# Performance work log

Measured on AMD Instinct MI355X. Metric: run time of the kernel, lower is better.

Reference implementation:

```python
import jax, jax.numpy as jnp
import numpy as np

# Fixed by JastrowNet source: ElectronicSchNet(n_interactions=2, kernel_dim=8, embedding_dim=16, version=1)
BATCH = 512
N_UP, N_DOWN = 16, 16
N_ELEC = N_UP + N_DOWN
N_ATOMS = 8
DIST_FEAT = 32
KERNEL = 8
EMBED = 16
N_LAYERS = 2
W_HIDDEN = 16  # log-spaced hidden dim of the w filter MLP: round(sqrt(32*8))
N_CHAN = 3     # same-spin, anti-spin, nuclear filter channels


def ssp(x):
    # shifted softplus used by SchNet
    return jax.nn.softplus(x) - jnp.log(2.0).astype(x.dtype)


def setup_inputs() -> dict:
    key = jax.random.key(0)
    ks = jax.random.split(key, 16)
    s = lambda fan_in: 1.0 / np.sqrt(fan_in)
    inp = {
        # Gaussian-expanded distance features are non-negative
        'edges_elec': jax.random.uniform(ks[0], (BATCH, N_ELEC, N_ELEC, DIST_FEAT), jnp.float32),
        'edges_nuc': jax.random.uniform(ks[1], (BATCH, N_ELEC, N_ATOMS, DIST_FEAT), jnp.float32),
        # electron spin embedding table (up=0, down=1) and nuclear embeddings Y
        'X_emb': jax.random.normal(ks[2], (2, EMBED), jnp.float32),
        'Y': jax.random.normal(ks[3], (N_ATOMS, KERNEL), jnp.float32),
        # per-layer, per-channel w filter MLP (dist_feat -> hidden -> kernel)
        'wW1': jax.random.normal(ks[4], (N_LAYERS, N_CHAN, DIST_FEAT, W_HIDDEN), jnp.float32) * s(DIST_FEAT),
        'wb1': jnp.zeros((N_LAYERS, N_CHAN, W_HIDDEN), jnp.float32),
        'wW2': jax.random.normal(ks[5], (N_LAYERS, N_CHAN, W_HIDDEN, KERNEL), jnp.float32) * s(W_HIDDEN),
        'wb2': jnp.zeros((N_LAYERS, N_CHAN, KERNEL), jnp.float32),
        # per-layer h subnet (embed -> kernel) and g subnet (kernel -> embed)
        'hW': jax.random.normal(ks[6], (N_LAYERS, EMBED, KERNEL), jnp.float32) * s(EMBED),
        'hb': jnp.zeros((N_LAYERS, KERNEL), jnp.float32),
        'gW': jax.random.normal(ks[7], (N_LAYERS, KERNEL, EMBED), jnp.float32) * s(KERNEL),
        'gb': jnp.zeros((N_LAYERS, EMBED), jnp.float32),
        # readout: Linear(16, 1, bias=False)
        'orb_W': jax.random.normal(ks[8], (EMBED,), jnp.float32) * s(EMBED),
    }
    return inp


def reference(edges_elec, edges_nuc, X_emb, Y, wW1, wb1, wW2, wb2, hW, hb, gW, gb, orb_W):
    B = edges_elec.shape[0]
    spins = jnp.concatenate([jnp.zeros(N_UP, jnp.int32), jnp.ones(N_DOWN, jnp.int32)])
    not_self = ~jnp.eye(N_ELEC, dtype=bool)
    same = ((spins[:, None] == spins[None, :]) & not_self)  # [n,n]
    anti = (spins[:, None] != spins[None, :])

    # initial electron embeddings by spin, broadcast over batch
    x = jnp.broadcast_to(X_emb[spins], (B, N_ELEC, EMBED))

    for l in range(N_LAYERS):
        def w_sub(e, c):
            h1 = ssp(e @ wW1[l, c] + wb1[l, c])
            return ssp(h1 @ wW2[l, c] + wb2[l, c])  # [..., KERNEL]

        w_same = w_sub(edges_elec, 0) * same[None, :, :, None]  # [B,n,n,k]
        w_anti = w_sub(edges_elec, 1) * anti[None, :, :, None]
        w_n = w_sub(edges_nuc, 2)                                # [B,n,m,k]

        hx = ssp(x @ hW[l] + hb[l])                              # [B,n,k]
        # continuous-filter message passing: gather neighbor features, multiply by filter, scatter-sum
        z = jnp.einsum('bijk,bjk->bik', w_same + w_anti, hx)
        z = z + jnp.einsum('bimk,mk->bik', w_n, Y)
        # version 1: single g applied to combined message, residual update
        x = x + z @ gW[l] + gb[l]

    # orbital readout Linear(16,1,bias=False).squeeze(-1).sum(-1)
    return (x @ orb_W).sum(axis=-1)  # [B]
```

## Files before the change

kernel.cpp:

```cpp
#include <hip/hip_runtime.h>
#include <hip/hip_bf16.h>
#include <cstddef>
#include <cstdint>


#define NB   512
#define NE   32
#define NA   8
#define NF   32
#define NH   16
#define NK   8
#define NEMB 16

typedef __attribute__((ext_vector_type(8))) short short8;
typedef __attribute__((ext_vector_type(4))) float f32x4;

__device__ __forceinline__ float ssp(float v){
    return fmaxf(v, 0.f) + __logf(1.f + __expf(-fabsf(v))) - 0.6931471805599453f;
}

__device__ __forceinline__ short f2bf(float x){
    unsigned b = __float_as_uint(x);
    b += 0x7fffu + ((b >> 16) & 1u);
    return (short)(b >> 16);
}
__device__ __forceinline__ unsigned packbf2(float lo, float hi){
    return (unsigned)(unsigned short)f2bf(lo) | ((unsigned)(unsigned short)f2bf(hi) << 16);
}
__device__ __forceinline__ short8 cvt_row(float4 a, float4 b){
    short8 s;
    s[0]=f2bf(a.x); s[1]=f2bf(a.y); s[2]=f2bf(a.z); s[3]=f2bf(a.w);
    s[4]=f2bf(b.x); s[5]=f2bf(b.y); s[6]=f2bf(b.z); s[7]=f2bf(b.w);
    return s;
}

extern "C" __global__ void __launch_bounds__(512, 4)
jastrow_kernel(const float* __restrict__ edges_elec,
               const float* __restrict__ edges_nuc,
               const float* __restrict__ X_emb,
               const float* __restrict__ Yk,
               const float* __restrict__ wW1, const float* __restrict__ wb1,
               const float* __restrict__ wW2, const float* __restrict__ wb2,
               const float* __restrict__ hW,  const float* __restrict__ hb,
               const float* __restrict__ gW,  const float* __restrict__ gb,
               const float* __restrict__ orbW,
               float* __restrict__ out)
{
    __shared__ __align__(16) __hip_bfloat16 s_w2[NE*NE*NK];
    __shared__ __align__(16) float s_z1p[2*NE*NK];
    __shared__ __align__(16) float s_zn1[NE*NK];
    __shared__ __align__(16) float s_zn2[NE*NK];
    __shared__ float s_hx1[2*NK];
    __shared__ float s_x[NE*NEMB];
    __shared__ float s_z[NE*NK];
    __shared__ float s_hx[NE*NK];
    __shared__ float s_red[8];

    const int b = blockIdx.x, t = threadIdx.x;
    const int wid = t >> 6, lane = t & 63;
    const int r16 = lane & 15, g4 = lane >> 4;

    if (t < 2*NK){
        const int s = t >> 3, k = t & 7;
        float acc = hb[k];
#pragma unroll
        for (int e = 0; e < NEMB; e++)
            acc = fmaf(X_emb[s*NEMB + e], hW[e*NK + k], acc);
        s_hx1[t] = ssp(acc);
    }
    __syncthreads();

    const int s0 = (g4*32 + r16) & 63;
    const int s1 = (g4*32 + 16 + r16) & 63;

    auto build = [&](int cc, short8* a1, short8* a2, f32x4* c1, f32x4* c2){
#pragma unroll
        for (int l = 0; l < 2; l++){
            const float* W1 = wW1 + (size_t)(l*3 + cc)*NF*NH;
            const float* W2 = wW2 + (size_t)(l*3 + cc)*NH*NK;
            short8 s, s2;
#pragma unroll
            for (int e = 0; e < 8; e++){
                s[e] = f2bf(W1[(g4*8 + e)*NH + r16]);
                const int h = g4*8 + e;
                s2[e] = (h < NH && r16 < NK) ? f2bf(W2[h*NK + r16]) : (short)0;
            }
            a1[l] = s; a2[l] = s2;
            const float* B1 = wb1 + (l*3 + cc)*NH;
            const float* B2 = wb2 + (l*3 + cc)*NK;
            f32x4 cb1, cb2;
#pragma unroll
            for (int r = 0; r < 4; r++){
                const int m = g4*4 + r;
                cb1[r] = B1[m];
                cb2[r] = (m < NK) ? B2[m] : 0.f;
            }
            c1[l] = cb1; c2[l] = cb2;
        }
    };

#pragma unroll
    for (int cc = 0; cc < 2; cc++){
        short8 a1[2], a2[2]; f32x4 c1[2], c2[2];
        build(cc, a1, a2, c1, c2);
#pragma unroll
        for (int u = 0; u < 4; u++){
            const int tau = wid*4 + u;
            const int qi = tau >> 4;
            const int qj = cc ? (1 - qi) : qi;
            const int g  = tau & 15;
            const int i  = qi*16 + g;
            const float* src = edges_elec
                + (((size_t)b*NE + i)*NE + qj*16 + r16)*NF + g4*8;
            const float4 ra = ((const float4*)src)[0];
            const float4 rb = ((const float4*)src)[1];
            const short8 bfr = cvt_row(ra, rb);
#pragma unroll
            for (int l = 0; l < 2; l++){
                f32x4 d1 = __builtin_amdgcn_mfma_f32_16x16x32_bf16(a1[l], bfr, c1[l], 0, 0, 0);
                const unsigned p0 = packbf2(ssp(d1[0]), ssp(d1[1]));
                const unsigned p1 = packbf2(ssp(d1[2]), ssp(d1[3]));
                unsigned q0 = __shfl(p0, s0, 64);
                unsigned q1 = __shfl(p1, s0, 64);
                unsigned q2 = __shfl(p0, s1, 64);
                unsigned q3 = __shfl(p1, s1, 64);
                if (g4 >= 2){ q0 = 0u; q1 = 0u; q2 = 0u; q3 = 0u; }
                union { unsigned u4[4]; short8 v; } bb;
                bb.u4[0]=q0; bb.u4[1]=q1; bb.u4[2]=q2; bb.u4[3]=q3;
                f32x4 d2 = __builtin_amdgcn_mfma_f32_16x16x32_bf16(a2[l], bb.v, c2[l], 0, 0, 0);
                float wk[4];
#pragma unroll
                for (int r = 0; r < 4; r++) wk[r] = ssp(d2[r]);
                if (cc == 0 && r16 == g){
#pragma unroll
                    for (int r = 0; r < 4; r++) wk[r] = 0.f;
                }
                if (l == 0){
#pragma unroll
                    for (int off = 1; off < 16; off <<= 1)
#pragma unroll
                        for (int r = 0; r < 4; r++) wk[r] += __shfl_xor(wk[r], off, 64);
                    if (r16 == 0 && g4 < 2){
                        float4 st;
                        st.x = wk[0]*s_hx1[qj*NK + g4*4 + 0];
                        st.y = wk[1]*s_hx1[qj*NK + g4*4 + 1];
                        st.z = wk[2]*s_hx1[qj*NK + g4*4 + 2];
                        st.w = wk[3]*s_hx1[qj*NK + g4*4 + 3];
                        *(float4*)&s_z1p[(qj*NE + i)*NK + g4*4] = st;
                    }
                } else if (g4 < 2){
                    const int j = qj*16 + r16;
                    uint2 uu;
                    uu.x = packbf2(wk[0], wk[1]);
                    uu.y = packbf2(wk[2], wk[3]);
                    *(uint2*)&s_w2[(i*NE + j)*NK + g4*4] = uu;
                }
            }
        }
    }

    {
        short8 a1[2], a2[2]; f32x4 c1[2], c2[2];
        build(2, a1, a2, c1, c2);
        const int m = lane & 7;
        float Yv[4];
#pragma unroll
        for (int r = 0; r < 4; r++)
            Yv[r] = Yk[m*NK + ((g4*4 + r) & 7)];
#pragma unroll
        for (int u = 0; u < 2; u++){
            const int gp = wid*2 + u;
            const int i  = 2*gp + (r16 >> 3);
            const float* src = edges_nuc
                + (((size_t)b*NE + i)*NA + m)*NF + g4*8;
            const float4 ra = ((const float4*)src)[0];
            const float4 rb = ((const float4*)src)[1];
            const short8 bfr = cvt_row(ra, rb);
#pragma unroll
            for (int l = 0; l < 2; l++){
                f32x4 d1 = __builtin_amdgcn_mfma_f32_16x16x32_bf16(a1[l], bfr, c1[l], 0, 0, 0);
                const unsigned p0 = packbf2(ssp(d1[0]), ssp(d1[1]));
                const unsigned p1 = packbf2(ssp(d1[2]), ssp(d1[3]));
                unsigned q0 = __shfl(p0, s0, 64);
                unsigned q1 = __shfl(p1, s0, 64);
                unsigned q2 = __shfl(p0, s1, 64);
                unsigned q3 = __shfl(p1, s1, 64);
                if (g4 >= 2){ q0 = 0u; q1 = 0u; q2 = 0u; q3 = 0u; }
                union { unsigned u4[4]; short8 v; } bb;
                bb.u4[0]=q0; bb.u4[1]=q1; bb.u4[2]=q2; bb.u4[3]=q3;
                f32x4 d2 = __builtin_amdgcn_mfma_f32_16x16x32_bf16(a2[l], bb.v, c2[l], 0, 0, 0);
                float wk[4];
#pragma unroll
                for (int r = 0; r < 4; r++) wk[r] = ssp(d2[r]) * Yv[r];
#pragma unroll
                for (int off = 1; off < 8; off <<= 1)
#pragma unroll
                    for (int r = 0; r < 4; r++) wk[r] += __shfl_xor(wk[r], off, 64);
                if ((r16 & 7) == 0 && g4 < 2){
                    float* dst = l ? s_zn2 : s_zn1;
                    float4 st; st.x = wk[0]; st.y = wk[1]; st.z = wk[2]; st.w = wk[3];
                    *(float4*)&dst[i*NK + g4*4] = st;
                }
            }
        }
    }
    __syncthreads();

    if (t < NE*NK)
        s_z[t] = s_z1p[t] + s_z1p[NE*NK + t] + s_zn1[t];
    __syncthreads();
    {
        const int i = t >> 4, e = t & 15;
        float acc = gb[e];
#pragma unroll
        for (int k = 0; k < NK; k++)
            acc = fmaf(s_z[i*NK + k], gW[k*NEMB + e], acc);
        s_x[t] = X_emb[(i >> 4)*NEMB + e] + acc;
    }
    __syncthreads();
    if (t < NE*NK){
        const int i = t >> 3, k = t & 7;
        float acc = hb[NK + k];
#pragma unroll
        for (int e = 0; e < NEMB; e++)
            acc = fmaf(s_x[i*NEMB + e], hW[NEMB*NK + e*NK + k], acc);
        s_hx[t] = ssp(acc);
    }
    __syncthreads();
    {
        const int i = t >> 4, j16 = t & 15;
        float zacc[NK];
#pragma unroll
        for (int k = 0; k < NK; k++) zacc[k] = 0.f;
#pragma unroll
        for (int qj = 0; qj < 2; qj++){
            const int j = qj*16 + j16;
            union { uint4 u; __hip_bfloat16 h[8]; } raw;
            raw.u = *(const uint4*)&s_w2[((size_t)i*NE + j)*NK];
            float pk[NK];
#pragma unroll
            for (int k = 0; k < NK; k++)
                pk[k] = __bfloat162float(raw.h[k]) * s_hx[j*NK + k];
#pragma unroll
            for (int off = 8; off > 0; off >>= 1)
#pragma unroll
                for (int k = 0; k < NK; k++) pk[k] += __shfl_down(pk[k], off, 16);
#pragma unroll
            for (int k = 0; k < NK; k++) zacc[k] += pk[k];
        }
        if (j16 == 0){
#pragma unroll
            for (int k = 0; k < NK; k++)
                s_z[i*NK + k] = zacc[k] + s_zn2[i*NK + k];
        }
    }
    __syncthreads();
    {
        const int i = t >> 4, e = t & 15;
        float acc = gb[NEMB + e];
#pragma unroll
        for (int k = 0; k < NK; k++)
            acc = fmaf(s_z[i*NK + k], gW[NK*NEMB + k*NEMB + e], acc);
        s_x[t] += acc;
    }
    __syncthreads();
    float part = s_x[t] * orbW[t & 15];
#pragma unroll
    for (int off = 32; off > 0; off >>= 1) part += __shfl_down(part, off, 64);
    if (lane == 0) s_red[wid] = part;
    __syncthreads();
    if (t == 0){
        float r = 0.f;
#pragma unroll
        for (int w = 0; w < 8; w++) r += s_red[w];
        out[b] = r;
    }
}

extern "C" void kernel_launch(void* const* d_in, const int* in_sizes, int n_in,
                              void* d_out, int out_size, void* d_ws, size_t ws_size,
                              hipStream_t stream)
{
    const float* edges_elec = (const float*)d_in[0];
    const float* edges_nuc  = (const float*)d_in[1];
    const float* X_emb      = (const float*)d_in[2];
    const float* Yk         = (const float*)d_in[3];
    const float* wW1        = (const float*)d_in[4];
    const float* wb1        = (const float*)d_in[5];
    const float* wW2        = (const float*)d_in[6];
    const float* wb2        = (const float*)d_in[7];
    const float* hW         = (const float*)d_in[8];
    const float* hb         = (const float*)d_in[9];
    const float* gW         = (const float*)d_in[10];
    const float* gb         = (const float*)d_in[11];
    const float* orbW       = (const float*)d_in[12];

    jastrow_kernel<<<NB, 512, 0, stream>>>(
        edges_elec, edges_nuc, X_emb, Yk, wW1, wb1, wW2, wb2, hW, hb,
        gW, gb, orbW, (float*)d_out);
}
```

Baseline: 156.2 us.

## Double block size, split filter channels across waves, use 16x16x16 second MFMA

Launches 1024 threads per block, with each wave handling a single electron filter channel. Each wave now processes four electron rows for one channel, and the nuclear pass covers one row pair. The second filter layer switches to the 16x16x16 bf16 MFMA, fed directly from per-lane ssp outputs, which removes the cross-lane shuffles and zero-padding that the K=32 instruction needed. The intent is more parallelism per batch item and fewer shuffle and ALU ops. The cost is more idle threads in the later per-electron phases and a larger block that may limit occupancy.

```diff
diff --git a/kernel.cpp b/kernel.cpp
--- a/kernel.cpp
+++ b/kernel.cpp
@@ -13,6 +13,7 @@
 #define NEMB 16
 
 typedef __attribute__((ext_vector_type(8))) short short8;
+typedef __attribute__((ext_vector_type(4))) short short4b;
 typedef __attribute__((ext_vector_type(4))) float f32x4;
 
 __device__ __forceinline__ float ssp(float v){
@@ -34,7 +35,18 @@
     return s;
 }
 
-extern "C" __global__ void __launch_bounds__(512, 4)
+__device__ __forceinline__ f32x4 mfma16x16(short4b a, short4b b, f32x4 c){
+#if __has_builtin(__builtin_amdgcn_mfma_f32_16x16x16bf16_1k)
+    return __builtin_amdgcn_mfma_f32_16x16x16bf16_1k(a, b, c, 0, 0, 0);
+#else
+    f32x4 d;
+    asm("s_nop 1\n\tv_mfma_f32_16x16x16_bf16 %0, %1, %2, %3\n\ts_nop 7"
+        : "=v"(d) : "v"(a), "v"(b), "v"(c));
+    return d;
+#endif
+}
+
+extern "C" __global__ void __launch_bounds__(1024, 8)
 jastrow_kernel(const float* __restrict__ edges_elec,
                const float* __restrict__ edges_nuc,
                const float* __restrict__ X_emb,
@@ -54,7 +66,7 @@
     __shared__ float s_x[NE*NEMB];
     __shared__ float s_z[NE*NK];
     __shared__ float s_hx[NE*NK];
-    __shared__ float s_red[8];
+    __shared__ float s_red[16];
 
     const int b = blockIdx.x, t = threadIdx.x;
     const int wid = t >> 6, lane = t & 63;
@@ -70,22 +82,22 @@
     }
     __syncthreads();
 
-    const int s0 = (g4*32 + r16) & 63;
-    const int s1 = (g4*32 + 16 + r16) & 63;
-
-    auto build = [&](int cc, short8* a1, short8* a2, f32x4* c1, f32x4* c2){
+    short8 a1[2]; short4b a2[2]; f32x4 c1[2], c2[2];
+    auto build = [&](int cc){
 #pragma unroll
         for (int l = 0; l < 2; l++){
             const float* W1 = wW1 + (size_t)(l*3 + cc)*NF*NH;
             const float* W2 = wW2 + (size_t)(l*3 + cc)*NH*NK;
-            short8 s, s2;
-#pragma unroll
-            for (int e = 0; e < 8; e++){
+            short8 s;
+#pragma unroll
+            for (int e = 0; e < 8; e++)
                 s[e] = f2bf(W1[(g4*8 + e)*NH + r16]);
-                const int h = g4*8 + e;
-                s2[e] = (h < NH && r16 < NK) ? f2bf(W2[h*NK + r16]) : (short)0;
-            }
-            a1[l] = s; a2[l] = s2;
+            a1[l] = s;
+            short4b s2;
+#pragma unroll
+            for (int e = 0; e < 4; e++)
+                s2[e] = (r16 < NK) ? f2bf(W2[(g4*4 + e)*NK + r16]) : (short)0;
+            a2[l] = s2;
             const float* B1 = wb1 + (l*3 + cc)*NH;
             const float* B2 = wb2 + (l*3 + cc)*NK;
             f32x4 cb1, cb2;
@@ -99,108 +111,92 @@
         }
     };
 
-#pragma unroll
-    for (int cc = 0; cc < 2; cc++){
-        short8 a1[2], a2[2]; f32x4 c1[2], c2[2];
-        build(cc, a1, a2, c1, c2);
-#pragma unroll
-        for (int u = 0; u < 4; u++){
-            const int tau = wid*4 + u;
-            const int qi = tau >> 4;
-            const int qj = cc ? (1 - qi) : qi;
-            const int g  = tau & 15;
-            const int i  = qi*16 + g;
-            const float* src = edges_elec
-                + (((size_t)b*NE + i)*NE + qj*16 + r16)*NF + g4*8;
-            const float4 ra = ((const float4*)src)[0];
-            const float4 rb = ((const float4*)src)[1];
-            const short8 bfr = cvt_row(ra, rb);
-#pragma unroll
-            for (int l = 0; l < 2; l++){
-                f32x4 d1 = __builtin_amdgcn_mfma_f32_16x16x32_bf16(a1[l], bfr, c1[l], 0, 0, 0);
-                const unsigned p0 = packbf2(ssp(d1[0]), ssp(d1[1]));
-                const unsigned p1 = packbf2(ssp(d1[2]), ssp(d1[3]));
-                unsigned q0 = __shfl(p0, s0, 64);
-                unsigned q1 = __shfl(p1, s0, 64);
-                unsigned q2 = __shfl(p0, s1, 64);
-                unsigned q3 = __shfl(p1, s1, 64);
-                if (g4 >= 2){ q0 = 0u; q1 = 0u; q2 = 0u; q3 = 0u; }
-                union { unsigned u4[4]; short8 v; } bb;
-                bb.u4[0]=q0; bb.u4[1]=q1; bb.u4[2]=q2; bb.u4[3]=q3;
-                f32x4 d2 = __builtin_amdgcn_mfma_f32_16x16x32_bf16(a2[l], bb.v, c2[l], 0, 0, 0);
-                float wk[4];
-#pragma unroll
-                for (int r = 0; r < 4; r++) wk[r] = ssp(d2[r]);
-                if (cc == 0 && r16 == g){
-#pragma unroll
-                    for (int r = 0; r < 4; r++) wk[r] = 0.f;
+    const int ccE = wid & 1;
+    const int wq  = (wid >> 1) * 4;
+    build(ccE);
+#pragma unroll
+    for (int u = 0; u < 4; u++){
+        const int tau = wq + u;
+        const int qi = tau >> 4, g = tau & 15;
+        const int qj = ccE ? (1 - qi) : qi;
+        const int i  = qi*16 + g;
+        const float* src = edges_elec
+            + (((size_t)b*NE + i)*NE + qj*16 + r16)*NF + g4*8;
+        const float4 ra = ((const float4*)src)[0];
+        const float4 rb = ((const float4*)src)[1];
+        const short8 bfr = cvt_row(ra, rb);
+#pragma unroll
+        for (int l = 0; l < 2; l++){
+            f32x4 d1 = __builtin_amdgcn_mfma_f32_16x16x32_bf16(a1[l], bfr, c1[l], 0, 0, 0);
+            short4b bb;
+            bb[0] = f2bf(ssp(d1[0]));
+            bb[1] = f2bf(ssp(d1[1]));
+            bb[2] = f2bf(ssp(d1[2]));
+            bb[3] = f2bf(ssp(d1[3]));
+            f32x4 d2 = mfma16x16(a2[l], bb, c2[l]);
+            float wk[4];
+#pragma unroll
+            for (int r = 0; r < 4; r++) wk[r] = ssp(d2[r]);
+            if (ccE == 0 && r16 == g){
+#pragma unroll
+                for (int r = 0; r < 4; r++) wk[r] = 0.f;
+            }
+            if (l == 0){
+#pragma unroll
+                for (int off = 1; off < 16; off <<= 1)
+#pragma unroll
+                    for (int r = 0; r < 4; r++) wk[r] += __shfl_xor(wk[r], off, 64);
+                if (r16 == 0 && g4 < 2){
+                    float4 st;
+                    st.x = wk[0]*s_hx1[qj*NK + g4*4 + 0];
+                    st.y = wk[1]*s_hx1[qj*NK + g4*4 + 1];
+                    st.z = wk[2]*s_hx1[qj*NK + g4*4 + 2];
+                    st.w = wk[3]*s_hx1[qj*NK + g4*4 + 3];
+                    *(float4*)&s_z1p[(qj*NE + i)*NK + g4*4] = st;
                 }
-                if (l == 0){
-#pragma unroll
-                    for (int off = 1; off < 16; off <<= 1)
-#pragma unroll
-                        for (int r = 0; r < 4; r++) wk[r] += __shfl_xor(wk[r], off, 64);
-                    if (r16 == 0 && g4 < 2){
-                        float4 st;
-                        st.x = wk[0]*s_hx1[qj*NK + g4*4 + 0];
-                        st.y = wk[1]*s_hx1[qj*NK + g4*4 + 1];
-                        st.z = wk[2]*s_hx1[qj*NK + g4*4 + 2];
-                        st.w = wk[3]*s_hx1[qj*NK + g4*4 + 3];
-                        *(float4*)&s_z1p[(qj*NE + i)*NK + g4*4] = st;
-                    }
-                } else if (g4 < 2){
-                    const int j = qj*16 + r16;
-                    uint2 uu;
-                    uu.x = packbf2(wk[0], wk[1]);
-                    uu.y = packbf2(wk[2], wk[3]);
-                    *(uint2*)&s_w2[(i*NE + j)*NK + g4*4] = uu;
-                }
+            } else if (g4 < 2){
+                const int j = qj*16 + r16;
+                uint2 uu;
+                uu.x = packbf2(wk[0], wk[1]);
+                uu.y = packbf2(wk[2], wk[3]);
+                *(uint2*)&s_w2[(i*NE + j)*NK + g4*4] = uu;
             }
         }
     }
 
     {
-        short8 a1[2], a2[2]; f32x4 c1[2], c2[2];
-        build(2, a1, a2, c1, c2);
+        build(2);
         const int m = lane & 7;
         float Yv[4];
 #pragma unroll
         for (int r = 0; r < 4; r++)
             Yv[r] = Yk[m*NK + ((g4*4 + r) & 7)];
-#pragma unroll
-        for (int u = 0; u < 2; u++){
-            const int gp = wid*2 + u;
-            const int i  = 2*gp + (r16 >> 3);
-            const float* src = edges_nuc
-                + (((size_t)b*NE + i)*NA + m)*NF + g4*8;
-            const float4 ra = ((const float4*)src)[0];
-            const float4 rb = ((const float4*)src)[1];
-            const short8 bfr = cvt_row(ra, rb);
-#pragma unroll
-            for (int l = 0; l < 2; l++){
-                f32x4 d1 = __builtin_amdgcn_mfma_f32_16x16x32_bf16(a1[l], bfr, c1[l], 0, 0, 0);
-                const unsigned p0 = packbf2(ssp(d1[0]), ssp(d1[1]));
-                const unsigned p1 = packbf2(ssp(d1[2]), ssp(d1[3]));
-                unsigned q0 = __shfl(p0, s0, 64);
-                unsigned q1 = __shfl(p1, s0, 64);
-                unsigned q2 = __shfl(p0, s1, 64);
-                unsigned q3 = __shfl(p1, s1, 64);
-                if (g4 >= 2){ q0 = 0u; q1 = 0u; q2 = 0u; q3 = 0u; }
-                union { unsigned u4[4]; short8 v; } bb;
-                bb.u4[0]=q0; bb.u4[1]=q1; bb.u4[2]=q2; bb.u4[3]=q3;
-                f32x4 d2 = __builtin_amdgcn_mfma_f32_16x16x32_bf16(a2[l], bb.v, c2[l], 0, 0, 0);
-                float wk[4];
-#pragma unroll
-                for (int r = 0; r < 4; r++) wk[r] = ssp(d2[r]) * Yv[r];
-#pragma unroll
-                for (int off = 1; off < 8; off <<= 1)
-#pragma unroll
-                    for (int r = 0; r < 4; r++) wk[r] += __shfl_xor(wk[r], off, 64);
-                if ((r16 & 7) == 0 && g4 < 2){
-                    float* dst = l ? s_zn2 : s_zn1;
-                    float4 st; st.x = wk[0]; st.y = wk[1]; st.z = wk[2]; st.w = wk[3];
-                    *(float4*)&dst[i*NK + g4*4] = st;
-                }
+        const int i = 2*wid + (r16 >> 3);
+        const float* src = edges_nuc
+            + (((size_t)b*NE + i)*NA + m)*NF + g4*8;
+        const float4 ra = ((const float4*)src)[0];
+        const float4 rb = ((const float4*)src)[1];
+        const short8 bfr = cvt_row(ra, rb);
+#pragma unroll
+        for (int l = 0; l < 2; l++){
+            f32x4 d1 = __builtin_amdgcn_mfma_f32_16x16x32_bf16(a1[l], bfr, c1[l], 0, 0, 0);
+            short4b bb;
+            bb[0] = f2bf(ssp(d1[0]));
+            bb[1] = f2bf(ssp(d1[1]));
+            bb[2] = f2bf(ssp(d1[2]));
+            bb[3] = f2bf(ssp(d1[3]));
+            f32x4 d2 = mfma16x16(a2[l], bb, c2[l]);
+            float wk[4];
+#pragma unroll
+            for (int r = 0; r < 4; r++) wk[r] = ssp(d2[r]) * Yv[r];
+#pragma unroll
+            for (int off = 1; off < 8; off <<= 1)
+#pragma unroll
+                for (int r = 0; r < 4; r++) wk[r] += __shfl_xor(wk[r], off, 64);
+            if ((r16 & 7) == 0 && g4 < 2){
+                float* dst = l ? s_zn2 : s_zn1;
+                float4 st; st.x = wk[0]; st.y = wk[1]; st.z = wk[2]; st.w = wk[3];
+                *(float4*)&dst[i*NK + g4*4] = st;
             }
         }
     }
@@ -209,7 +205,7 @@
     if (t < NE*NK)
         s_z[t] = s_z1p[t] + s_z1p[NE*NK + t] + s_zn1[t];
     __syncthreads();
-    {
+    if (t < NE*NEMB){
         const int i = t >> 4, e = t & 15;
         float acc = gb[e];
 #pragma unroll
@@ -227,7 +223,7 @@
         s_hx[t] = ssp(acc);
     }
     __syncthreads();
-    {
+    if (t < NE*NEMB){
         const int i = t >> 4, j16 = t & 15;
         float zacc[NK];
 #pragma unroll
@@ -255,7 +251,7 @@
         }
     }
     __syncthreads();
-    {
+    if (t < NE*NEMB){
         const int i = t >> 4, e = t & 15;
         float acc = gb[NEMB + e];
 #pragma unroll
@@ -264,7 +260,7 @@
         s_x[t] += acc;
     }
     __syncthreads();
-    float part = s_x[t] * orbW[t & 15];
+    float part = (t < NE*NEMB) ? s_x[t] * orbW[t & 15] : 0.f;
 #pragma unroll
     for (int off = 32; off > 0; off >>= 1) part += __shfl_down(part, off, 64);
     if (lane == 0) s_red[wid] = part;
@@ -272,7 +268,7 @@
     if (t == 0){
         float r = 0.f;
 #pragma unroll
-        for (int w = 0; w < 8; w++) r += s_red[w];
+        for (int w = 0; w < 16; w++) r += s_red[w];
         out[b] = r;
     }
 }
@@ -295,7 +291,7 @@
     const float* gb         = (const float*)d_in[11];
     const float* orbW       = (const float*)d_in[12];
 
-    jastrow_kernel<<<NB, 512, 0, stream>>>(
+    jastrow_kernel<<<NB, 1024, 0, stream>>>(
         edges_elec, edges_nuc, X_emb, Yk, wW1, wb1, wW2, wb2, hW, hb,
         gW, gb, orbW, (float*)d_out);
 }
```

New measurement: 154.2 us. No clear change (-1.2%).
